# Optimization experiments

Measured on AMD Instinct MI355X. Metric: run time of the kernel, lower is better.

The kernel has to match this reference:

```python
import jax, jax.numpy as jnp
import numpy as np

N_U = 20000; N_I = 20000; D = 256
NNZ = 600000; EGG = 300000; EDD = 300000; B = 8192
DROP = 0.1; LAM2 = 1e-7


def _attention(x, W, a, edges):
    # GAT-style attention over sampled relationship edges (src -> tgt).
    n, d = x.shape
    h = x @ W                                  # [n, d]
    src, tgt = edges[0], edges[1]
    e = jax.nn.leaky_relu((h @ a[:d])[src] + (h @ a[d:])[tgt], 0.2)  # [E]
    m = jax.ops.segment_max(e, tgt, num_segments=n)
    m = jnp.where(jnp.isfinite(m), m, 0.0)
    ex = jnp.exp(e - m[tgt])
    denom = jax.ops.segment_sum(ex, tgt, num_segments=n)             # [n]
    num = jax.ops.segment_sum(ex[:, None] * h[src], tgt, num_segments=n)  # [n, d]
    return num / (denom[:, None] + 1e-9)


def _spmm(rows, cols, vals, x, n_out):
    # sparse [n_out, n_in] @ dense [n_in, d]
    return jax.ops.segment_sum(vals[:, None] * x[cols], rows, num_segments=n_out)


def _mlp(x, W1, b1, W2, b2, W3, b3):
    h = jax.nn.relu(x @ W1 + b1)
    h = jax.nn.relu(h @ W2 + b2)
    return (h @ W3 + b3)[..., 0]


def setup_inputs() -> dict:
    key = jax.random.key(0)
    ks = jax.random.split(key, 24)
    s = 0.02
    inp = {
        'E_g_0': jax.random.normal(ks[0], (N_U, D), jnp.float32) * s,
        'E_d_0': jax.random.normal(ks[1], (N_I, D), jnp.float32) * s,
        'att_W': jax.random.normal(ks[2], (D, D), jnp.float32) * s,
        'att_a': jax.random.normal(ks[3], (2 * D,), jnp.float32) * s,
        'att1_W': jax.random.normal(ks[4], (D, D), jnp.float32) * s,
        'att1_a': jax.random.normal(ks[5], (2 * D,), jnp.float32) * s,
        'W1': jax.random.normal(ks[6], (2 * D, D), jnp.float32) * s,
        'b1': jnp.zeros((D,), jnp.float32),
        'W2': jax.random.normal(ks[7], (D, D), jnp.float32) * s,
        'b2': jnp.zeros((D,), jnp.float32),
        'W3': jax.random.normal(ks[8], (D, 1), jnp.float32) * s,
        'b3': jnp.zeros((1,), jnp.float32),
        'M1': jax.random.normal(ks[9], (2 * D, D), jnp.float32) * s,
        'mb1': jnp.zeros((D,), jnp.float32),
        'M2': jax.random.normal(ks[10], (D, D), jnp.float32) * s,
        'mb2': jnp.zeros((D,), jnp.float32),
        'adj_vals': jax.random.uniform(ks[11], (NNZ,), jnp.float32),
        'uids': jax.random.randint(ks[12], (B,), 0, N_U, jnp.int32),
        'iids': jax.random.randint(ks[13], (B,), 0, N_I, jnp.int32),
        'pos': jax.random.randint(ks[14], (B,), 0, N_I, jnp.int32),
        'neg': jax.random.randint(ks[15], (B,), 0, N_I, jnp.int32),
        'gene_edges': jax.random.randint(ks[16], (2, EGG), 0, N_U, jnp.int32),
        'drug_edges': jax.random.randint(ks[17], (2, EDD), 0, N_I, jnp.int32),
        'adj_rows': jax.random.randint(ks[18], (NNZ,), 0, N_U, jnp.int32),
        'adj_cols': jax.random.randint(ks[19], (NNZ,), 0, N_I, jnp.int32),
        'drop1': jax.random.bernoulli(ks[20], 1.0 - DROP, (NNZ,)),
        'drop2': jax.random.bernoulli(ks[21], 1.0 - DROP, (NNZ,)),
    }
    return inp


def reference(E_g_0, E_d_0, att_W, att_a, att1_W, att1_a, W1, b1, W2, b2, W3, b3,
              M1, mb1, M2, mb2, adj_vals, uids, iids, pos, neg,
              gene_edges, drug_edges, adj_rows, adj_cols, drop1, drop2):
    # Attention-modulated layer-0 embeddings
    E_d0 = 0.1 * _attention(E_d_0, att_W, att_a, drug_edges) + E_d_0
    E_g0 = 0.1 * _attention(E_g_0, att_W, att_a, gene_edges) + E_g_0

    # sparse_dropout + spmm (two independent dropout draws, as in the source)
    scale = 1.0 / (1.0 - DROP)
    v1 = adj_vals * drop1.astype(adj_vals.dtype) * scale
    v2 = adj_vals * drop2.astype(adj_vals.dtype) * scale
    E_g = _spmm(adj_rows, adj_cols, v1, E_d0, N_U)   # adj @ E_d0
    E_d = _spmm(adj_cols, adj_rows, v2, E_g0, N_I)   # adj.T @ E_g0

    u = E_g[uids]; p = E_d[pos]; ng = E_d[neg]
    pos_s = _mlp(jnp.concatenate([u, p], axis=-1), W1, b1, W2, b2, W3, b3)
    neg_s = _mlp(jnp.concatenate([u, ng], axis=-1), W1, b1, W2, b2, W3, b3)

    # BCE-with-logits (labels 1 for pos, 0 for neg) + BPR term
    loss_pos = jnp.mean(jax.nn.softplus(-pos_s))
    loss_neg = jnp.mean(jax.nn.softplus(neg_s))
    loss_bpr = jnp.mean(jax.nn.softplus(-(pos_s - neg_s)))
    loss_r = loss_pos + loss_neg + loss_bpr

    params = (E_g_0, E_d_0, att_W, att_a, att1_W, att1_a,
              W1, b1, W2, b2, W3, b3, M1, mb1, M2, mb2)
    loss_reg = LAM2 * sum(jnp.sum(p_ * p_) for p_ in params)

    loss = loss_reg + loss_r  # loss_s == 0
    return jnp.stack([loss, loss_r, jnp.zeros((), loss.dtype)])
```

## Files before the change

### kernel.cpp

```cpp
#include <hip/hip_runtime.h>
#include <math.h>

#define N_NODES 20000
#define D       256
#define NNZ     600000
#define NEDGE   300000
#define BATCH   8192
#define DROP_SCALE (1.0f/0.9f)
#define LAM2_F  1e-7f

#define M_PAD   20096
#define CSTRIDE 20032

#define C_ATT 56
#define C_ADJ 80

#define BINW 320
#define NBIN 63
#define TILE_E 2048
#define EPT 8
#define T_ATT ((NEDGE + TILE_E - 1) / TILE_E)
#define T_ADJ ((NNZ + TILE_E - 1) / TILE_E)
#define NBLK_P1 (2 * T_ATT + 2 * T_ADJ)
#define CAP_BIN_ATT 5376
#define CAP_BIN_ADJ 6144

#define FP8_SCALE 256.0f
#define VSCALE    58980.0f
#define INV_VSCALE (1.0f/58980.0f)

typedef unsigned short u16;
typedef unsigned char  u8;
typedef __attribute__((ext_vector_type(8))) short bf16x8;
typedef __attribute__((ext_vector_type(4))) float f32x4;
typedef __attribute__((ext_vector_type(2))) float f32x2;
typedef __attribute__((ext_vector_type(4))) unsigned v4u;

__device__ inline float wave_reduce(float v) {
    #pragma unroll
    for (int off = 32; off > 0; off >>= 1) v += __shfl_down(v, off, 64);
    return v;
}

__device__ inline float softplus_f(float x) {
    float r = log1pf(__expf(-fabsf(x)));
    return x > 0.f ? x + r : r;
}

__device__ inline u16 f2bf(float f) {
    unsigned u = __float_as_uint(f);
    unsigned r = u + 0x7fff + ((u >> 16) & 1);
    return (u16)(r >> 16);
}
__device__ inline float bf2f(u16 b) { return __uint_as_float(((unsigned)b) << 16); }

__device__ inline u16 f2h(float f) {
    _Float16 h = (_Float16)f;
    return __builtin_bit_cast(u16, h);
}
__device__ inline float h2f(u16 b) {
    return (float)__builtin_bit_cast(_Float16, b);
}

__device__ inline unsigned f32x4_to_fp8x4(float a, float b, float c, float d) {
    int r = 0;
    r = __builtin_amdgcn_cvt_pk_fp8_f32(a, b, r, false);
    r = __builtin_amdgcn_cvt_pk_fp8_f32(c, d, r, true);
    return (unsigned)r;
}
__device__ inline u8 f32_to_fp8(float a) {
    int r = __builtin_amdgcn_cvt_pk_fp8_f32(a, a, 0, false);
    return (u8)(r & 0xff);
}

__device__ inline void gld_lds16(const void* g, void* l) {
    __builtin_amdgcn_global_load_lds((const __attribute__((address_space(1))) void*)g,
                                     (__attribute__((address_space(3))) void*)l, 16, 0, 0);
}

struct RegArgs { const float* p[14]; int n[14]; };

__global__ __launch_bounds__(256) void init_kernel(const unsigned char* __restrict__ drop,
                                                   const int* __restrict__ uids, const int* __restrict__ pos,
                                                   const int* __restrict__ neg,
                                                   const float* __restrict__ att_W, const float* __restrict__ att_a,
                                                   float* __restrict__ wlv, float* __restrict__ wrv,
                                                   unsigned* __restrict__ bm2, unsigned* __restrict__ bm3,
                                                   unsigned int* __restrict__ flag) {
    if (blockIdx.x < 96) {
        int i = blockIdx.x * blockDim.x + threadIdx.x;
        if (i < BATCH) {
            int v = uids[i];
            atomicOr(&bm2[v >> 5], 1u << (v & 31));
        } else if (i < 2 * BATCH) {
            int v = pos[i - BATCH];
            atomicOr(&bm3[v >> 5], 1u << (v & 31));
        } else {
            int v = neg[i - 2 * BATCH];
            atomicOr(&bm3[v >> 5], 1u << (v & 31));
        }
    } else if (blockIdx.x == 96) {
        __shared__ int cnt_s;
        if (threadIdx.x == 0) cnt_s = 0;
        __syncthreads();
        int c = 0;
        for (int i = threadIdx.x; i < 1024; i += blockDim.x)
            if (drop[4*i + 1] != 0) c++;
        atomicAdd(&cnt_s, c);
        __syncthreads();
        if (threadIdx.x == 0) *flag = (cnt_s > 64) ? 1u : 0u;
    } else {
        int t = threadIdx.x;
        float s1 = 0.f, s2 = 0.f;
        for (int n = 0; n < D; n++) {
            float w = att_W[(size_t)t * D + n];
            s1 += w * att_a[n];
            s2 += w * att_a[D + n];
        }
        wlv[t] = s1; wrv[t] = s2;
    }
}

#define NB_CAST (2 * M_PAD / 4)
#define NB_T1   (D * D / 256)
#define NB_T2   (2 * D * D / 256)
#define NB_T3   (D * D / 256)
#define NB_PREP (NB_CAST + NB_T1 + NB_T2 + NB_T3)
#define NB_REG  448
__global__ __launch_bounds__(256) void p1prep_kernel(
        const int* __restrict__ dtgt, const int* __restrict__ dsrc,
        const int* __restrict__ gtgt, const int* __restrict__ gsrc,
        const int* __restrict__ ar,   const int* __restrict__ ac,
        const float* __restrict__ vals,
        const void* __restrict__ drop1, const void* __restrict__ drop2,
        const unsigned int* __restrict__ flag,
        const unsigned* __restrict__ bm2, const unsigned* __restrict__ bm3,
        int* __restrict__ pcur, unsigned* __restrict__ attbin, uint2* __restrict__ adjbin,
        const float* __restrict__ E_g, const float* __restrict__ E_d,
        u16* __restrict__ Eg_bf, u16* __restrict__ Ed_bf,
        const float* __restrict__ att_W,
        const float* __restrict__ W1, const float* __restrict__ W2,
        u16* __restrict__ attWT, u16* __restrict__ W1T, u16* __restrict__ W2T,
        const float* __restrict__ wlv, const float* __restrict__ wrv,
        float* __restrict__ hl_g, float* __restrict__ hr_g,
        float* __restrict__ hl_d, float* __restrict__ hr_d,
        float* __restrict__ regp, RegArgs ra, float* __restrict__ acc) {
    if (blockIdx.x < NBLK_P1) {
        __shared__ int hist[NBIN];
        __shared__ int basep[NBIN];
        for (int i = threadIdx.x; i < NBIN; i += 256) hist[i] = 0;
        __syncthreads();

        int b = blockIdx.x;
        int s, t0;
        if (b < T_ATT)               { s = 0; t0 = b; }
        else if (b < 2 * T_ATT)      { s = 1; t0 = b - T_ATT; }
        else if (b < 2*T_ATT + T_ADJ){ s = 2; t0 = b - 2 * T_ATT; }
        else                         { s = 3; t0 = b - 2 * T_ATT - T_ADJ; }
        int base = t0 * TILE_E;
        int regN = (s < 2) ? NEDGE : NNZ;

        int bins[EPT], rank[EPT];
        unsigned key[EPT], pay[EPT];
        float pv[EPT];

        if (s < 2) {
            const int* tgt = (s == 0) ? dtgt : gtgt;
            const int* src = (s == 0) ? dsrc : gsrc;
            #pragma unroll
            for (int e = 0; e < EPT; e++) {
                int idx = base + e * 256 + threadIdx.x;
                rank[e] = -1;
                if (idx < regN) {
                    int k = __builtin_nontemporal_load(tgt + idx);
                    int sv = __builtin_nontemporal_load(src + idx);
                    key[e] = (unsigned)k; pay[e] = (unsigned)sv;
                    bins[e] = k / BINW;
                    rank[e] = atomicAdd(&hist[bins[e]], 1);
                }
            }
        } else {
            const unsigned int bf = *flag;
            const int* keyp = (s == 2) ? ar : ac;
            const int* othp = (s == 2) ? ac : ar;
            const void* drp = (s == 2) ? drop1 : drop2;
            const unsigned* bm = (s == 2) ? bm2 : bm3;
            #pragma unroll
            for (int e = 0; e < EPT; e++) {
                int idx = base + e * 256 + threadIdx.x;
                rank[e] = -1;
                if (idx < regN) {
                    int k = __builtin_nontemporal_load(keyp + idx);
                    if ((bm[k >> 5] >> (k & 31)) & 1) {
                        bool keep = bf ? (__builtin_nontemporal_load((const u8*)drp + idx) != 0)
                                       : (__builtin_nontemporal_load((const unsigned*)drp + idx) != 0);
                        if (keep) {
                            float v = __builtin_nontemporal_load(vals + idx) * DROP_SCALE;
                            int oth = __builtin_nontemporal_load(othp + idx);
                            key[e] = (unsigned)k; pay[e] = (unsigned)oth; pv[e] = v;
                            bins[e] = k / BINW;
                            rank[e] = atomicAdd(&hist[bins[e]], 1);
                        }
                    }
                }
            }
        }
        __syncthreads();
        for (int i = threadIdx.x; i < NBIN; i += 256) {
            int h = hist[i];
            basep[i] = h ? atomicAdd(&pcur[s * NBIN + i], h) : 0;
        }
        __syncthreads();
        if (s < 2) {
            unsigned* seg = attbin + (size_t)s * NBIN * CAP_BIN_ATT;
            #pragma unroll
            for (int e = 0; e < EPT; e++) {
                if (rank[e] < 0) continue;
                int pos = basep[bins[e]] + rank[e];
                if (pos < CAP_BIN_ATT)
                    seg[(size_t)bins[e] * CAP_BIN_ATT + pos] = key[e] | (pay[e] << 16);
            }
        } else {
            uint2* seg = adjbin + (size_t)(s - 2) * NBIN * CAP_BIN_ADJ;
            #pragma unroll
            for (int e = 0; e < EPT; e++) {
                if (rank[e] < 0) continue;
                int pos = basep[bins[e]] + rank[e];
                if (pos < CAP_BIN_ADJ) {
                    uint2 pr; pr.x = key[e] | (pay[e] << 16); pr.y = __float_as_uint(pv[e]);
                    seg[(size_t)bins[e] * CAP_BIN_ADJ + pos] = pr;
                }
            }
        }
    } else {
        int bid = blockIdx.x - NBLK_P1;
        int w = threadIdx.x >> 6, lane = threadIdx.x & 63;
        if (bid < NB_CAST) {
            int wid  = (bid * 256 + threadIdx.x) >> 6;
            int is_d = (wid >= M_PAD);
            int row  = is_d ? wid - M_PAD : wid;
            u16* dst = (is_d ? Ed_bf : Eg_bf) + (size_t)row * D;
            float s3 = 0.f;
            if (row >= N_NODES) {
                ((ushort4*)dst)[lane] = make_ushort4(0, 0, 0, 0);
            } else {
                const float* src = (is_d ? E_d : E_g) + (size_t)row * D;
                float4 e  = ((const float4*)src)[lane];
                float4 l4 = ((const float4*)wlv)[lane];
                float4 r4 = ((const float4*)wrv)[lane];
                ((ushort4*)dst)[lane] = make_ushort4(f2bf(e.x), f2bf(e.y), f2bf(e.z), f2bf(e.w));
                float s1 = e.x*l4.x + e.y*l4.y + e.z*l4.z + e.w*l4.w;
                float s2 = e.x*r4.x + e.y*r4.y + e.z*r4.z + e.w*r4.w;
                s3 = e.x*e.x + e.y*e.y + e.z*e.z + e.w*e.w;
                s1 = wave_reduce(s1); s2 = wave_reduce(s2);
                if (lane == 0) {
                    if (is_d) { hl_d[row] = s1; hr_d[row] = s2; }
                    else      { hl_g[row] = s1; hr_g[row] = s2; }
                }
            }
            s3 = wave_reduce(s3);
            __shared__ float sm3[4];
            if (lane == 0) sm3[threadIdx.x >> 6] = s3;
            __syncthreads();
            if (threadIdx.x == 0) regp[bid] = sm3[0] + sm3[1] + sm3[2] + sm3[3];
        } else if (bid < NB_CAST + NB_T1) {
            int o = (bid - NB_CAST) * 256 + threadIdx.x;
            int n = o >> 8, k = o & 255;
            attWT[o] = f2bf(att_W[(size_t)k * D + n]);
        } else if (bid < NB_CAST + NB_T1 + NB_T2) {
            int o = (bid - NB_CAST - NB_T1) * 256 + threadIdx.x;
            int n = o / (2 * D), k = o - n * (2 * D);
            W1T[o] = f2bf(W1[(size_t)k * D + n]);
        } else if (bid < NB_PREP) {
            int o = (bid - NB_CAST - NB_T1 - NB_T2) * 256 + threadIdx.x;
            int n = o >> 8, k = o & 255;
            W2T[o] = f2bf(W2[(size_t)k * D + n]);
        } else {
            int rb = bid - NB_PREP;
            const float* p = ra.p[rb >> 5];
            int n = ra.n[rb >> 5];
            int base = (rb & 31) * 4096;
            if (base >= n) return;
            float sum = 0.f;
            if (base + 4096 <= n) {
                const float4* p4 = (const float4*)(p + base);
                float4 v = p4[threadIdx.x];
                sum += v.x*v.x + v.y*v.y + v.z*v.z + v.w*v.w;
                v = p4[256 + threadIdx.x];
                sum += v.x*v.x + v.y*v.y + v.z*v.z + v.w*v.w;
                v = p4[512 + threadIdx.x];
                sum += v.x*v.x + v.y*v.y + v.z*v.z + v.w*v.w;
                v = p4[768 + threadIdx.x];
                sum += v.x*v.x + v.y*v.y + v.z*v.z + v.w*v.w;
            } else {
                for (int i = base + threadIdx.x; i < n; i += 256) { float v = p[i]; sum += v * v; }
            }
            sum = wave_reduce(sum);
            __shared__ float smr[4];
            if (lane == 0) smr[w] = sum;
            __syncthreads();
            if (threadIdx.x == 0)
                atomicAdd(&acc[0], smr[0] + smr[1] + smr[2] + smr[3]);
        }
    }
}

#define NB_P2   (4 * NBIN)
#define NB_ATTG ((M_PAD / 128) * 4)
__global__ __launch_bounds__(256) void p2gemm_kernel(
        const int* __restrict__ pcur, const unsigned* __restrict__ attbin,
        const uint2* __restrict__ adjbin,
        const float* __restrict__ hl_d, const float* __restrict__ hr_d,
        const float* __restrict__ hl_g, const float* __restrict__ hr_g,
        int* __restrict__ cnt, unsigned* __restrict__ srcs, unsigned* __restrict__ adj,
        const u16* __restrict__ Eg_bf, const u16* __restrict__ Ed_bf,
        const u16* __restrict__ attWT, u8* __restrict__ h_g, u8* __restrict__ h_d) {
    if (blockIdx.x < NB_P2) {
        int s   = blockIdx.x / NBIN;
        int bin = blockIdx.x - s * NBIN;
        int nodeBase = bin * BINW;
        __shared__ int cur[BINW];
        for (int t = threadIdx.x; t < BINW; t += 256) cur[t] = 0;
        __syncthreads();
        if (s < 2) {
            int m = pcur[s * NBIN + bin]; if (m > CAP_BIN_ATT) m = CAP_BIN_ATT;
            const unsigned* seg = attbin + ((size_t)s * NBIN + bin) * CAP_BIN_ATT;
            const float* hl = (s == 0) ? hl_d : hl_g;
            const float* hr = (s == 0) ? hr_d : hr_g;
            for (int k = threadIdx.x; k < m; k += 256) {
                unsigned e = seg[k];
                int lk  = (int)(e & 0xFFFFu) - nodeBase;
                int src = (int)(e >> 16);
                float ev = hl[src] + hr[nodeBase + lk];
                ev = ev > 0.f ? ev : 0.2f * ev;
                u16 xh = f2h(__expf(ev));
                int c = atomicAdd(&cur[lk], 1);
                if (c < C_ATT)
                    srcs[(size_t)s * N_NODES * C_ATT + (size_t)(nodeBase + lk) * C_ATT + c] =
                        (unsigned)src | ((unsigned)xh << 16);
            }
            __syncthreads();
            for (int t = threadIdx.x; t < BINW; t += 256) {
                int node = nodeBase + t;
                if (node < N_NODES) {
                    int n = cur[t]; if (n > C_ATT) n = C_ATT;
                    cnt[s * CSTRIDE + node] = n;
                }
            }
        } else {
            int m = pcur[s * NBIN + bin]; if (m > CAP_BIN_ADJ) m = CAP_BIN_ADJ;
            const uint2* seg = adjbin + ((size_t)(s - 2) * NBIN + bin) * CAP_BIN_ADJ;
            for (int k = threadIdx.x; k < m; k += 256) {
                uint2 e = seg[k];
                int lk  = (int)(e.x & 0xFFFFu) - nodeBase;
                int oth = (int)(e.x >> 16);
                float v = __uint_as_float(e.y);
                unsigned pk = ((unsigned)(v * VSCALE + 0.5f) << 16) | (unsigned)oth;
                int c = atomicAdd(&cur[lk], 1);
                if (c < C_ADJ)
                    adj[(size_t)(s - 2) * N_NODES * C_ADJ + (size_t)(nodeBase + lk) * C_ADJ + c] = pk;
            }
            __syncthreads();
            for (int t = threadIdx.x; t < BINW; t += 256) {
                int node = nodeBase + t;
                if (node < N_NODES) {
                    int n = cur[t]; if (n > C_ADJ) n = C_ADJ;
                    cnt[s * CSTRIDE + node] = n;
                }
            }
        }
    } else {
        int t  = blockIdx.x - NB_P2;
        int z  = t / (2 * (M_PAD / 128));
        int r  = t - z * (2 * (M_PAD / 128));
        int by = r / (M_PAD / 128);
        int bx = r - by * (M_PAD / 128);
        const u16* A = z ? Ed_bf : Eg_bf;
        u8* C = z ? h_d : h_g;
        __shared__ __align__(16) short As[128][32];
        __shared__ __align__(16) short Bs[128][32];
        int tid = threadIdx.x;
        int wave = tid >> 6, lane = tid & 63;
        int bm = bx * 128, bn = by * 128;
        int sr = lane >> 2;
        int sc = (lane & 3) * 8;

        f32x4 acc[4][4];
        #pragma unroll
        for (int i = 0; i < 4; i++)
            #pragma unroll
            for (int j = 0; j < 4; j++)
                #pragma unroll
                for (int q = 0; q < 4; q++) acc[i][j][q] = 0.f;

        int wr = (wave >> 1) * 64;
        int wc = (wave & 1) * 64;
        int fr = lane & 15;
        int fk = (lane >> 4) * 8;

        for (int k0 = 0; k0 < D; k0 += 32) {
            #pragma unroll
            for (int j = 0; j < 2; j++) {
                int r0 = wave * 32 + j * 16;
                gld_lds16(A     + (size_t)(bm + r0 + sr) * D + k0 + sc, &As[r0][0]);
                gld_lds16(attWT + (size_t)(bn + r0 + sr) * D + k0 + sc, &Bs[r0][0]);
            }
            __syncthreads();
            bf16x8 af[4], bfr[4];
            #pragma unroll
            for (int i = 0; i < 4; i++) af[i]  = *(const bf16x8*)&As[wr + i*16 + fr][fk];
            #pragma unroll
            for (int j = 0; j < 4; j++) bfr[j] = *(const bf16x8*)&Bs[wc + j*16 + fr][fk];
            #pragma unroll
            for (int i = 0; i < 4; i++)
                #pragma unroll
                for (int j = 0; j < 4; j++)
                    acc[i][j] = __builtin_amdgcn_mfma_f32_16x16x32_bf16(af[i], bfr[j], acc[i][j], 0, 0, 0);
            __syncthreads();
        }

        #pragma unroll
        for (int j = 0; j < 4; j++) {
            int col = bn + wc + j * 16 + fr;
            #pragma unroll
            for (int i = 0; i < 4; i++) {
                #pragma unroll
                for (int q = 0; q < 4; q++) {
                    int row = bm + wr + i * 16 + (lane >> 4) * 4 + q;
                    if (row < N_NODES)
                        C[(size_t)row * D + col] = f32_to_fp8(acc[i][j][q] * FP8_SCALE);
                }
            }
        }
    }
}

__global__ __launch_bounds__(256) void gemm_bf16(const u16* __restrict__ A, const u16* __restrict__ BT,
                                                 void* __restrict__ C, int M, int N, int K,
                                                 const float* __restrict__ bias, int do_relu, int out_mode,
                                                 const float* __restrict__ w3) {
    __shared__ __align__(16) short As[128][32];
    __shared__ __align__(16) short Bs[128][32];
    int tid = threadIdx.x;
    int wave = tid >> 6, lane = tid & 63;
    int bm = blockIdx.x * 128, bn = blockIdx.y * 128;
    int sr = lane >> 2;
    int sc = (lane & 3) * 8;

    f32x4 acc[4][4];
    #pragma unroll
    for (int i = 0; i < 4; i++)
        #pragma unroll
        for (int j = 0; j < 4; j++)
            #pragma unroll
            for (int r = 0; r < 4; r++) acc[i][j][r] = 0.f;

    int wr = (wave >> 1) * 64;
    int wc = (wave & 1) * 64;
    int fr = lane & 15;
    int fk = (lane >> 4) * 8;

    for (int k0 = 0; k0 < K; k0 += 32) {
        #pragma unroll
        for (int j = 0; j < 2; j++) {
            int r0 = wave * 32 + j * 16;
            gld_lds16(A  + (size_t)(bm + r0 + sr) * K + k0 + sc, &As[r0][0]);
            gld_lds16(BT + (size_t)(bn + r0 + sr) * K + k0 + sc, &Bs[r0][0]);
        }
        __syncthreads();
        bf16x8 af[4], bfr[4];
        #pragma unroll
        for (int i = 0; i < 4; i++) af[i]  = *(const bf16x8*)&As[wr + i*16 + fr][fk];
        #pragma unroll
        for (int j = 0; j < 4; j++) bfr[j] = *(const bf16x8*)&Bs[wc + j*16 + fr][fk];
        #pragma unroll
        for (int i = 0; i < 4; i++)
            #pragma unroll
            for (int j = 0; j < 4; j++)
                acc[i][j] = __builtin_amdgcn_mfma_f32_16x16x32_bf16(af[i], bfr[j], acc[i][j], 0, 0, 0);
        __syncthreads();
    }

    if (out_mode == 2) {
        __shared__ float sacc[128];
        for (int t = tid; t < 128; t += 256) sacc[t] = 0.f;
        __syncthreads();
        float bvj[4], w3j[4];
        #pragma unroll
        for (int j = 0; j < 4; j++) {
            int col = bn + wc + j * 16 + fr;
            bvj[j] = bias[col];
            w3j[j] = w3[col];
        }
        #pragma unroll
        for (int i = 0; i < 4; i++) {
            #pragma unroll
            for (int r = 0; r < 4; r++) {
                float rs = 0.f;
                #pragma unroll
                for (int j = 0; j < 4; j++) {
                    float v = fmaxf(acc[i][j][r] + bvj[j], 0.f);
                    rs += v * w3j[j];
                }
                rs += __shfl_xor(rs, 1, 64);
                rs += __shfl_xor(rs, 2, 64);
                rs += __shfl_xor(rs, 4, 64);
                rs += __shfl_xor(rs, 8, 64);
                if (fr == 0)
                    atomicAdd(&sacc[wr + i * 16 + (lane >> 4) * 4 + r], rs);
            }
        }
        __syncthreads();
        float* sb = (float*)C;
        for (int t = tid; t < 128; t += 256)
            atomicAdd(&sb[bm + t], sacc[t]);
        return;
    }

    #pragma unroll
    for (int j = 0; j < 4; j++) {
        int col = bn + wc + j * 16 + fr;
        float bv = bias ? bias[col] : 0.f;
        #pragma unroll
        for (int i = 0; i < 4; i++) {
            #pragma unroll
            for (int r = 0; r < 4; r++) {
                int row = bm + wr + i * 16 + (lane >> 4) * 4 + r;
                if (row < M) {
                    float v = acc[i][j][r] + bv;
                    if (do_relu) v = fmaxf(v, 0.f);
                    ((u16*)C)[(size_t)row * N + col] = f2bf(v);
                }
            }
        }
    }
}

__global__ __launch_bounds__(256) void att_kernel(const u8* __restrict__ h_d, const u8* __restrict__ h_g,
                                                  const int* __restrict__ cur, const unsigned* __restrict__ srcs,
                                                  const u16* __restrict__ Ed_bf, const u16* __restrict__ Eg_bf,
                                                  u8* __restrict__ E_d0p, u8* __restrict__ E_g0p) {
    int wid  = (blockIdx.x * blockDim.x + threadIdx.x) >> 6;
    int lane = threadIdx.x & 63;
    if (wid >= 2 * N_NODES) return;
    int is_g = (wid >= N_NODES);
    int node = is_g ? wid - N_NODES : wid;
    const unsigned* h32 = (const unsigned*)(is_g ? h_g : h_d);
    int reg = is_g ? 1 : 0;
    const unsigned* sv = srcs + (size_t)reg * N_NODES * C_ATT + (size_t)node * C_ATT;
    int n = cur[reg * CSTRIDE + node];
    if (n > C_ATT) n = C_ATT;
    float ax = 0.f, ay = 0.f, az = 0.f, aw = 0.f, denom = 0.f;
    int k = 0;
    for (; k + 8 <= n; k += 8) {
        v4u qa = __builtin_nontemporal_load((const v4u*)(sv + k));
        v4u qb = __builtin_nontemporal_load((const v4u*)(sv + k + 4));
        unsigned g[8]; float x[8];
        #pragma unroll
        for (int j = 0; j < 4; j++) {
            g[j]     = h32[((size_t)(qa[j] & 0xFFFFu) << 6) + lane];
            g[4 + j] = h32[((size_t)(qb[j] & 0xFFFFu) << 6) + lane];
            x[j]     = h2f((u16)(qa[j] >> 16));
            x[4 + j] = h2f((u16)(qb[j] >> 16));
        }
        #pragma unroll
        for (int j = 0; j < 8; j++) {
            denom += x[j];
            f32x2 lo = __builtin_amdgcn_cvt_pk_f32_fp8(g[j], false);
            f32x2 hi = __builtin_amdgcn_cvt_pk_f32_fp8(g[j], true);
            ax += x[j]*lo[0]; ay += x[j]*lo[1]; az += x[j]*hi[0]; aw += x[j]*hi[1];
        }
    }
    for (; k + 4 <= n; k += 4) {
        v4u qa = __builtin_nontemporal_load((const v4u*)(sv + k));
        unsigned g[4]; float x[4];
        #pragma unroll
        for (int j = 0; j < 4; j++) {
            g[j] = h32[((size_t)(qa[j] & 0xFFFFu) << 6) + lane];
            x[j] = h2f((u16)(qa[j] >> 16));
        }
        #pragma unroll
        for (int j = 0; j < 4; j++) {
            denom += x[j];
            f32x2 lo = __builtin_amdgcn_cvt_pk_f32_fp8(g[j], false);
            f32x2 hi = __builtin_amdgcn_cvt_pk_f32_fp8(g[j], true);
            ax += x[j]*lo[0]; ay += x[j]*lo[1]; az += x[j]*hi[0]; aw += x[j]*hi[1];
        }
    }
    for (; k < n; k++) {
        unsigned q = sv[k];
        float xv = h2f((u16)(q >> 16));
        unsigned g = h32[((size_t)(q & 0xFFFFu) << 6) + lane];
        denom += xv;
        f32x2 lo = __builtin_amdgcn_cvt_pk_f32_fp8(g, false);
        f32x2 hi = __builtin_amdgcn_cvt_pk_f32_fp8(g, true);
        ax += xv*lo[0]; ay += xv*lo[1]; az += xv*hi[0]; aw += xv*hi[1];
    }
    float sc = 0.1f / (denom + 1e-9f);
    const u16* E0b = is_g ? Eg_bf : Ed_bf;
    u8*       out  = is_g ? E_g0p : E_d0p;
    ushort4 b4 = ((const ushort4*)(E0b + (size_t)node * D))[lane];
    unsigned pk = f32x4_to_fp8x4(FP8_SCALE * bf2f(b4.x) + sc * ax, FP8_SCALE * bf2f(b4.y) + sc * ay,
                                 FP8_SCALE * bf2f(b4.z) + sc * az, FP8_SCALE * bf2f(b4.w) + sc * aw);
    ((unsigned*)(out + (size_t)node * D))[lane] = pk;
}

__global__ __launch_bounds__(256) void pull_kernel(const int* __restrict__ uids, const int* __restrict__ pos,
                                                   const int* __restrict__ neg,
                                                   const int* __restrict__ cur, const unsigned* __restrict__ adj,
                                                   const u8* __restrict__ E_d0p, const u8* __restrict__ E_g0p,
                                                   u16* __restrict__ X) {
    int wid  = (blockIdx.x * blockDim.x + threadIdx.x) >> 6;
    int lane = threadIdx.x & 63;
    if (wid >= 3 * BATCH) return;
    int type = wid >> 13;
    int b    = wid & (BATCH - 1);
    int node, reg; const u8* E;
    if (type == 0)      { node = uids[b]; reg = 2; E = E_d0p; }
    else if (type == 1) { node = pos[b];  reg = 3; E = E_g0p; }
    else                { node = neg[b];  reg = 3; E = E_g0p; }
    const unsigned* E32 = (const unsigned*)E;
    const unsigned* av = adj + (size_t)(reg - 2) * N_NODES * C_ADJ + (size_t)node * C_ADJ;
    int n = cur[reg * CSTRIDE + node];
    if (n > C_ADJ) n = C_ADJ;
    float ax = 0.f, ay = 0.f, az = 0.f, aw = 0.f;
    int k = 0;
    for (; k + 8 <= n; k += 8) {
        v4u qa = __builtin_nontemporal_load((const v4u*)(av + k));
        v4u qb = __builtin_nontemporal_load((const v4u*)(av + k + 4));
        unsigned g[8]; float v[8];
        #pragma unroll
        for (int j = 0; j < 4; j++) {
            g[j]     = E32[((size_t)(qa[j] & 0xFFFFu) << 6) + lane];
            g[4 + j] = E32[((size_t)(qb[j] & 0xFFFFu) << 6) + lane];
            v[j]     = (float)(qa[j] >> 16) * INV_VSCALE;
            v[4 + j] = (float)(qb[j] >> 16) * INV_VSCALE;
        }
        #pragma unroll
        for (int j = 0; j < 8; j++) {
            f32x2 lo = __builtin_amdgcn_cvt_pk_f32_fp8(g[j], false);
            f32x2 hi = __builtin_amdgcn_cvt_pk_f32_fp8(g[j], true);
            ax += v[j]*lo[0]; ay += v[j]*lo[1]; az += v[j]*hi[0]; aw += v[j]*hi[1];
        }
    }
    for (; k + 4 <= n; k += 4) {
        v4u qa = __builtin_nontemporal_load((const v4u*)(av + k));
        unsigned g[4]; float v[4];
        #pragma unroll
        for (int j = 0; j < 4; j++) {
            g[j] = E32[((size_t)(qa[j] & 0xFFFFu) << 6) + lane];
            v[j] = (float)(qa[j] >> 16) * INV_VSCALE;
        }
        #pragma unroll
        for (int j = 0; j < 4; j++) {
            f32x2 lo = __builtin_amdgcn_cvt_pk_f32_fp8(g[j], false);
            f32x2 hi = __builtin_amdgcn_cvt_pk_f32_fp8(g[j], true);
            ax += v[j]*lo[0]; ay += v[j]*lo[1]; az += v[j]*hi[0]; aw += v[j]*hi[1];
        }
    }
    for (; k < n; k++) {
        unsigned q = av[k];
        int c = q & 0xFFFF;
        float v = (float)(q >> 16) * INV_VSCALE;
        unsigned g = E32[((size_t)c << 6) + lane];
        f32x2 lo = __builtin_amdgcn_cvt_pk_f32_fp8(g, false);
        f32x2 hi = __builtin_amdgcn_cvt_pk_f32_fp8(g, true);
        ax += v*lo[0]; ay += v*lo[1]; az += v*hi[0]; aw += v*hi[1];
    }
    const float inv = 1.0f / FP8_SCALE;
    ushort4 r = make_ushort4(f2bf(ax * inv), f2bf(ay * inv), f2bf(az * inv), f2bf(aw * inv));
    if (type == 0) {
        ((ushort4*)(X + (size_t)b * 2 * D))[lane] = r;
        ((ushort4*)(X + (size_t)(BATCH + b) * 2 * D))[lane] = r;
    } else if (type == 1) {
        ((ushort4*)(X + (size_t)b * 2 * D + D))[lane] = r;
    } else {
        ((ushort4*)(X + (size_t)(BATCH + b) * 2 * D + D))[lane] = r;
    }
}

#define NB_TAIL 16
__global__ __launch_bounds__(256) void tail_kernel(const float* __restrict__ s,
                                                   const float* __restrict__ b3p,
                                                   const float* __restrict__ regp,
                                                   float* __restrict__ acc, float* __restrict__ out) {
    int bid = blockIdx.x, tid = threadIdx.x;
    int w = tid >> 6, lane = tid & 63;
    float b3 = b3p[0];
    float lp = 0.f, ln = 0.f, lb = 0.f, rsum = 0.f;
    for (int i = bid * 256 + tid; i < BATCH; i += NB_TAIL * 256) {
        float ps = s[i] + b3, ns = s[BATCH + i] + b3;
        lp += softplus_f(-ps);
        ln += softplus_f(ns);
        lb += softplus_f(-(ps - ns));
    }
    for (int i = bid * 256 + tid; i < NB_CAST; i += NB_TAIL * 256) rsum += regp[i];
    lp = wave_reduce(lp); ln = wave_reduce(ln); lb = wave_reduce(lb); rsum = wave_reduce(rsum);
    __shared__ float sm[4][4];
    if (lane == 0) { sm[0][w] = lp; sm[1][w] = ln; sm[2][w] = lb; sm[3][w] = rsum; }
    __syncthreads();
    if (tid == 0) {
        float a = 0.f, b = 0.f, c = 0.f, rg = 0.f;
        for (int i = 0; i < 4; i++) { a += sm[0][i]; b += sm[1][i]; c += sm[2][i]; rg += sm[3][i]; }
        atomicAdd(&acc[1], a); atomicAdd(&acc[2], b); atomicAdd(&acc[3], c);
        atomicAdd(&acc[0], rg);
    }
    __syncthreads();
    __shared__ int lastf;
    if (tid == 0) {
        __threadfence();
        unsigned t = atomicAdd((unsigned*)&acc[8], 1u);
        lastf = (t == NB_TAIL - 1);
    }
    __syncthreads();
    if (!lastf || tid != 0) return;
    float a0 = __hip_atomic_load(&acc[0], __ATOMIC_RELAXED, __HIP_MEMORY_SCOPE_AGENT);
    float a1 = __hip_atomic_load(&acc[1], __ATOMIC_RELAXED, __HIP_MEMORY_SCOPE_AGENT);
    float a2 = __hip_atomic_load(&acc[2], __ATOMIC_RELAXED, __HIP_MEMORY_SCOPE_AGENT);
    float a3 = __hip_atomic_load(&acc[3], __ATOMIC_RELAXED, __HIP_MEMORY_SCOPE_AGENT);
    float lr = (a1 + a2 + a3) * (1.0f / (float)BATCH);
    out[0] = LAM2_F * a0 + lr;
    out[1] = lr;
    out[2] = 0.f;
}

extern "C" void kernel_launch(void* const* d_in, const int* in_sizes, int n_in,
                              void* d_out, int out_size, void* d_ws, size_t ws_size,
                              hipStream_t stream) {
    (void)n_in; (void)out_size; (void)ws_size;
    const float* E_g_0   = (const float*)d_in[0];
    const float* E_d_0   = (const float*)d_in[1];
    const float* att_W   = (const float*)d_in[2];
    const float* att_a   = (const float*)d_in[3];
    const float* W1      = (const float*)d_in[6];
    const float* b1      = (const float*)d_in[7];
    const float* W2      = (const float*)d_in[8];
    const float* b2      = (const float*)d_in[9];
    const float* W3      = (const float*)d_in[10];
    const float* b3      = (const float*)d_in[11];
    const float* adj_vals= (const float*)d_in[16];
    const int*   uids    = (const int*)d_in[17];
    const int*   pos     = (const int*)d_in[19];
    const int*   neg     = (const int*)d_in[20];
    const int*   gene_e  = (const int*)d_in[21];
    const int*   drug_e  = (const int*)d_in[22];
    const int*   adj_rows= (const int*)d_in[23];
    const int*   adj_cols= (const int*)d_in[24];
    const void*  drop1   = d_in[25];
    const void*  drop2   = d_in[26];

    char* ws = (char*)d_ws;
    size_t cur_off = 0;
    auto take = [&](size_t bytes) -> void* {
        void* p = ws + cur_off;
        cur_off += (bytes + 255) & ~(size_t)255;
        return p;
    };
    u16* Eg_bf = (u16*)take((size_t)M_PAD * D * 2);
    u16* Ed_bf = (u16*)take((size_t)M_PAD * D * 2);
    u16* X     = Eg_bf;
    u16* attWT = (u16*)take((size_t)D * D * 2);
    u16* W1T   = (u16*)take((size_t)D * 2 * D * 2);
    u16* W2T   = (u16*)take((size_t)D * D * 2);
    u8*  h_g   = (u8*)take((size_t)M_PAD * D);
    u8*  h_d   = (u8*)take((size_t)M_PAD * D);
    u8*  E_g0p = (u8*)take((size_t)N_NODES * D);
    u8*  E_d0p = (u8*)take((size_t)N_NODES * D);
    u16* H1    = (u16*)take((size_t)2 * BATCH * D * 2);
    float* hl_g = (float*)take((size_t)N_NODES * 4);
    float* hr_g = (float*)take((size_t)N_NODES * 4);
    float* hl_d = (float*)take((size_t)N_NODES * 4);
    float* hr_d = (float*)take((size_t)N_NODES * 4);
    float* wlv  = (float*)take((size_t)D * 4);
    float* wrv  = (float*)take((size_t)D * 4);
    float* regp = (float*)take((size_t)NB_CAST * 4);
    unsigned* srcs = (unsigned*)take((size_t)2 * N_NODES * C_ATT * 4);
    unsigned* adj  = (unsigned*)take((size_t)2 * N_NODES * C_ADJ * 4);
    int*   cnt  = (int*)take((size_t)4 * CSTRIDE * 4);
    unsigned* attbin = (unsigned*)take((size_t)2 * NBIN * CAP_BIN_ATT * 4);
    uint2*    adjbin = (uint2*)take((size_t)2 * NBIN * CAP_BIN_ADJ * 8);
    int*      pcur = (int*)take((size_t)4 * NBIN * 4);
    unsigned* bm2  = (unsigned*)take(4096);
    unsigned* bm3  = (unsigned*)take(4096);
    float*    acc  = (float*)take(256);
    float*    sbuf = (float*)take((size_t)2 * BATCH * 4);
    size_t zbytes = (char*)sbuf + (size_t)2 * BATCH * 4 - (char*)pcur;

    hipMemsetAsync(pcur, 0, zbytes, stream);
    init_kernel<<<98, 256, 0, stream>>>((const unsigned char*)drop1, uids, pos, neg,
                                        att_W, att_a, wlv, wrv,
                                        bm2, bm3, (unsigned int*)(acc + 4));

    RegArgs ra;
    for (int i = 0; i < 14; i++) { ra.p[i] = (const float*)d_in[i + 2]; ra.n[i] = in_sizes[i + 2]; }
    p1prep_kernel<<<NBLK_P1 + NB_PREP + NB_REG, 256, 0, stream>>>(
        drug_e + NEDGE, drug_e, gene_e + NEDGE, gene_e,
        adj_rows, adj_cols, adj_vals, drop1, drop2,
        (const unsigned int*)(acc + 4), bm2, bm3,
        pcur, attbin, adjbin,
        E_g_0, E_d_0, Eg_bf, Ed_bf, att_W, W1, W2,
        attWT, W1T, W2T, wlv, wrv, hl_g, hr_g, hl_d, hr_d, regp, ra, acc);

    p2gemm_kernel<<<NB_P2 + NB_ATTG, 256, 0, stream>>>(
        pcur, attbin, adjbin, hl_d, hr_d, hl_g, hr_g, cnt, srcs, adj,
        Eg_bf, Ed_bf, attWT, h_g, h_d);

    att_kernel<<<10000, 256, 0, stream>>>(h_d, h_g, cnt, srcs,
                                          Ed_bf, Eg_bf, E_d0p, E_g0p);

    pull_kernel<<<6144, 256, 0, stream>>>(uids, pos, neg, cnt, adj, E_d0p, E_g0p, X);

    gemm_bf16<<<dim3(2 * BATCH / 128, 2, 1), 256, 0, stream>>>(
        X, W1T, H1, 2 * BATCH, D, 2 * D, b1, 1, 0, nullptr);
    gemm_bf16<<<dim3(2 * BATCH / 128, 2, 1), 256, 0, stream>>>(
        H1, W2T, sbuf, 2 * BATCH, D, D, b2, 1, 2, W3);

    tail_kernel<<<NB_TAIL, 256, 0, stream>>>(sbuf, b3, regp, acc, (float*)d_out);
}
```

Measured before the change: 297.6 us.

## Fuse MLP GEMMs and loss tail into one kernel, drop batch bitmaps

The two MLP GEMM launches and the loss tail launch are merged into a single kernel. Its stages are chained by per-row-tile atomic counters with spin-waits. The memset and the bitmap/flag init work are folded into a single-block init kernel that zeroes the scratch and computes the attention projection vectors. The adjacency binning no longer filters edges by the uid/pos/neg bitmaps, so every kept edge is binned, and the bin capacity is raised to fit. The dropout-format detection moves into each block via a ballot. This removes launches and bitmap work but adds more binned edges, and the spin-waits depend on the producer blocks being scheduled before the consumers.

```diff
diff --git a/kernel.cpp b/kernel.cpp
--- a/kernel.cpp
+++ b/kernel.cpp
@@ -23,7 +23,7 @@
 #define T_ADJ ((NNZ + TILE_E - 1) / TILE_E)
 #define NBLK_P1 (2 * T_ATT + 2 * T_ADJ)
 #define CAP_BIN_ATT 5376
-#define CAP_BIN_ADJ 6144
+#define CAP_BIN_ADJ 9216
 
 #define FP8_SCALE 256.0f
 #define VSCALE    58980.0f
@@ -80,44 +80,54 @@
 
 struct RegArgs { const float* p[14]; int n[14]; };
 
-__global__ __launch_bounds__(256) void init_kernel(const unsigned char* __restrict__ drop,
-                                                   const int* __restrict__ uids, const int* __restrict__ pos,
-                                                   const int* __restrict__ neg,
-                                                   const float* __restrict__ att_W, const float* __restrict__ att_a,
-                                                   float* __restrict__ wlv, float* __restrict__ wrv,
-                                                   unsigned* __restrict__ bm2, unsigned* __restrict__ bm3,
-                                                   unsigned int* __restrict__ flag) {
-    if (blockIdx.x < 96) {
-        int i = blockIdx.x * blockDim.x + threadIdx.x;
-        if (i < BATCH) {
-            int v = uids[i];
-            atomicOr(&bm2[v >> 5], 1u << (v & 31));
-        } else if (i < 2 * BATCH) {
-            int v = pos[i - BATCH];
-            atomicOr(&bm3[v >> 5], 1u << (v & 31));
-        } else {
-            int v = neg[i - 2 * BATCH];
-            atomicOr(&bm3[v >> 5], 1u << (v & 31));
-        }
-    } else if (blockIdx.x == 96) {
-        __shared__ int cnt_s;
-        if (threadIdx.x == 0) cnt_s = 0;
-        __syncthreads();
-        int c = 0;
-        for (int i = threadIdx.x; i < 1024; i += blockDim.x)
-            if (drop[4*i + 1] != 0) c++;
-        atomicAdd(&cnt_s, c);
-        __syncthreads();
-        if (threadIdx.x == 0) *flag = (cnt_s > 64) ? 1u : 0u;
-    } else {
-        int t = threadIdx.x;
-        float s1 = 0.f, s2 = 0.f;
-        for (int n = 0; n < D; n++) {
-            float w = att_W[(size_t)t * D + n];
-            s1 += w * att_a[n];
-            s2 += w * att_a[D + n];
-        }
-        wlv[t] = s1; wrv[t] = s2;
+__device__ inline void gemm_tile_k(const u16* __restrict__ A, const u16* __restrict__ BT, int K,
+                                   int bm, int bn, short (*As)[32], short (*Bs)[32],
+                                   f32x4 (&acr)[4][4]) {
+    int tid = threadIdx.x, wave = tid >> 6, lane = tid & 63;
+    int sr = lane >> 2, sc = (lane & 3) * 8;
+    int wr = (wave >> 1) * 64, wc = (wave & 1) * 64;
+    int fr = lane & 15, fk = (lane >> 4) * 8;
+    for (int k0 = 0; k0 < K; k0 += 32) {
+        #pragma unroll
+        for (int j = 0; j < 2; j++) {
+            int r0 = wave * 32 + j * 16;
+            gld_lds16(A  + (size_t)(bm + r0 + sr) * K + k0 + sc, &As[r0][0]);
+            gld_lds16(BT + (size_t)(bn + r0 + sr) * K + k0 + sc, &Bs[r0][0]);
+        }
+        __syncthreads();
+        bf16x8 af[4], bfr[4];
+        #pragma unroll
+        for (int i = 0; i < 4; i++) af[i]  = *(const bf16x8*)&As[wr + i*16 + fr][fk];
+        #pragma unroll
+        for (int j = 0; j < 4; j++) bfr[j] = *(const bf16x8*)&Bs[wc + j*16 + fr][fk];
+        #pragma unroll
+        for (int i = 0; i < 4; i++)
+            #pragma unroll
+            for (int j = 0; j < 4; j++)
+                acr[i][j] = __builtin_amdgcn_mfma_f32_16x16x32_bf16(af[i], bfr[j], acr[i][j], 0, 0, 0);
+        __syncthreads();
+    }
+}
+
+__global__ __launch_bounds__(1024) void init_kernel(const float* __restrict__ att_W,
+                                                    const float* __restrict__ att_a,
+                                                    float* __restrict__ wlv, float* __restrict__ wrv,
+                                                    int* __restrict__ zbase, int zwords) {
+    int tid = threadIdx.x;
+    for (int i = tid; i < zwords; i += 1024) zbase[i] = 0;
+    int t = tid & 255, q = tid >> 8;
+    float s1 = 0.f, s2 = 0.f;
+    for (int n = q * 64; n < q * 64 + 64; n++) {
+        float w = att_W[(size_t)t * D + n];
+        s1 += w * att_a[n];
+        s2 += w * att_a[D + n];
+    }
+    __shared__ float r1[4][256], r2[4][256];
+    r1[q][t] = s1; r2[q][t] = s2;
+    __syncthreads();
+    if (q == 0) {
+        wlv[t] = r1[0][t] + r1[1][t] + r1[2][t] + r1[3][t];
+        wrv[t] = r2[0][t] + r2[1][t] + r2[2][t] + r2[3][t];
     }
 }
 
@@ -133,8 +143,6 @@
         const int* __restrict__ ar,   const int* __restrict__ ac,
         const float* __restrict__ vals,
         const void* __restrict__ drop1, const void* __restrict__ drop2,
-        const unsigned int* __restrict__ flag,
-        const unsigned* __restrict__ bm2, const unsigned* __restrict__ bm3,
         int* __restrict__ pcur, unsigned* __restrict__ attbin, uint2* __restrict__ adjbin,
         const float* __restrict__ E_g, const float* __restrict__ E_d,
         u16* __restrict__ Eg_bf, u16* __restrict__ Ed_bf,
@@ -180,27 +188,25 @@
                 }
             }
         } else {
-            const unsigned int bf = *flag;
             const int* keyp = (s == 2) ? ar : ac;
             const int* othp = (s == 2) ? ac : ar;
             const void* drp = (s == 2) ? drop1 : drop2;
-            const unsigned* bm = (s == 2) ? bm2 : bm3;
+            bool nzs = ((const u8*)drp)[4 * threadIdx.x + 1] != 0;
+            const bool bf = __popcll(__ballot(nzs)) > 16;
             #pragma unroll
             for (int e = 0; e < EPT; e++) {
                 int idx = base + e * 256 + threadIdx.x;
                 rank[e] = -1;
                 if (idx < regN) {
-                    int k = __builtin_nontemporal_load(keyp + idx);
-                    if ((bm[k >> 5] >> (k & 31)) & 1) {
-                        bool keep = bf ? (__builtin_nontemporal_load((const u8*)drp + idx) != 0)
-                                       : (__builtin_nontemporal_load((const unsigned*)drp + idx) != 0);
-                        if (keep) {
-                            float v = __builtin_nontemporal_load(vals + idx) * DROP_SCALE;
-                            int oth = __builtin_nontemporal_load(othp + idx);
-                            key[e] = (unsigned)k; pay[e] = (unsigned)oth; pv[e] = v;
-                            bins[e] = k / BINW;
-                            rank[e] = atomicAdd(&hist[bins[e]], 1);
-                        }
+                    bool keep = bf ? (__builtin_nontemporal_load((const u8*)drp + idx) != 0)
+                                   : (__builtin_nontemporal_load((const unsigned*)drp + idx) != 0);
+                    if (keep) {
+                        int k = __builtin_nontemporal_load(keyp + idx);
+                        float v = __builtin_nontemporal_load(vals + idx) * DROP_SCALE;
+                        int oth = __builtin_nontemporal_load(othp + idx);
+                        key[e] = (unsigned)k; pay[e] = (unsigned)oth; pv[e] = v;
+                        bins[e] = k / BINW;
+                        rank[e] = atomicAdd(&hist[bins[e]], 1);
                     }
                 }
             }
@@ -379,46 +385,17 @@
         u8* C = z ? h_d : h_g;
         __shared__ __align__(16) short As[128][32];
         __shared__ __align__(16) short Bs[128][32];
-        int tid = threadIdx.x;
-        int wave = tid >> 6, lane = tid & 63;
+        int wave = threadIdx.x >> 6, lane = threadIdx.x & 63;
         int bm = bx * 128, bn = by * 128;
-        int sr = lane >> 2;
-        int sc = (lane & 3) * 8;
-
-        f32x4 acc[4][4];
+        f32x4 acr[4][4];
         #pragma unroll
         for (int i = 0; i < 4; i++)
             #pragma unroll
             for (int j = 0; j < 4; j++)
                 #pragma unroll
-                for (int q = 0; q < 4; q++) acc[i][j][q] = 0.f;
-
-        int wr = (wave >> 1) * 64;
-        int wc = (wave & 1) * 64;
-        int fr = lane & 15;
-        int fk = (lane >> 4) * 8;
-
-        for (int k0 = 0; k0 < D; k0 += 32) {
-            #pragma unroll
-            for (int j = 0; j < 2; j++) {
-                int r0 = wave * 32 + j * 16;
-                gld_lds16(A     + (size_t)(bm + r0 + sr) * D + k0 + sc, &As[r0][0]);
-                gld_lds16(attWT + (size_t)(bn + r0 + sr) * D + k0 + sc, &Bs[r0][0]);
-            }
-            __syncthreads();
-            bf16x8 af[4], bfr[4];
-            #pragma unroll
-            for (int i = 0; i < 4; i++) af[i]  = *(const bf16x8*)&As[wr + i*16 + fr][fk];
-            #pragma unroll
-            for (int j = 0; j < 4; j++) bfr[j] = *(const bf16x8*)&Bs[wc + j*16 + fr][fk];
-            #pragma unroll
-            for (int i = 0; i < 4; i++)
-                #pragma unroll
-                for (int j = 0; j < 4; j++)
-                    acc[i][j] = __builtin_amdgcn_mfma_f32_16x16x32_bf16(af[i], bfr[j], acc[i][j], 0, 0, 0);
-            __syncthreads();
-        }
-
+                for (int q = 0; q < 4; q++) acr[i][j][q] = 0.f;
+        gemm_tile_k(A, attWT, D, bm, bn, As, Bs, acr);
+        int wr = (wave >> 1) * 64, wc = (wave & 1) * 64, fr = lane & 15;
         #pragma unroll
         for (int j = 0; j < 4; j++) {
             int col = bn + wc + j * 16 + fr;
@@ -428,108 +405,7 @@
                 for (int q = 0; q < 4; q++) {
                     int row = bm + wr + i * 16 + (lane >> 4) * 4 + q;
                     if (row < N_NODES)
-                        C[(size_t)row * D + col] = f32_to_fp8(acc[i][j][q] * FP8_SCALE);
-                }
-            }
-        }
-    }
-}
-
-__global__ __launch_bounds__(256) void gemm_bf16(const u16* __restrict__ A, const u16* __restrict__ BT,
-                                                 void* __restrict__ C, int M, int N, int K,
-                                                 const float* __restrict__ bias, int do_relu, int out_mode,
-                                                 const float* __restrict__ w3) {
-    __shared__ __align__(16) short As[128][32];
-    __shared__ __align__(16) short Bs[128][32];
-    int tid = threadIdx.x;
-    int wave = tid >> 6, lane = tid & 63;
-    int bm = blockIdx.x * 128, bn = blockIdx.y * 128;
-    int sr = lane >> 2;
-    int sc = (lane & 3) * 8;
-
-    f32x4 acc[4][4];
-    #pragma unroll
-    for (int i = 0; i < 4; i++)
-        #pragma unroll
-        for (int j = 0; j < 4; j++)
-            #pragma unroll
-            for (int r = 0; r < 4; r++) acc[i][j][r] = 0.f;
-
-    int wr = (wave >> 1) * 64;
-    int wc = (wave & 1) * 64;
-    int fr = lane & 15;
-    int fk = (lane >> 4) * 8;
-
-    for (int k0 = 0; k0 < K; k0 += 32) {
-        #pragma unroll
-        for (int j = 0; j < 2; j++) {
-            int r0 = wave * 32 + j * 16;
-            gld_lds16(A  + (size_t)(bm + r0 + sr) * K + k0 + sc, &As[r0][0]);
-            gld_lds16(BT + (size_t)(bn + r0 + sr) * K + k0 + sc, &Bs[r0][0]);
-        }
-        __syncthreads();
-        bf16x8 af[4], bfr[4];
-        #pragma unroll
-        for (int i = 0; i < 4; i++) af[i]  = *(const bf16x8*)&As[wr + i*16 + fr][fk];
-        #pragma unroll
-        for (int j = 0; j < 4; j++) bfr[j] = *(const bf16x8*)&Bs[wc + j*16 + fr][fk];
-        #pragma unroll
-        for (int i = 0; i < 4; i++)
-            #pragma unroll
-            for (int j = 0; j < 4; j++)
-                acc[i][j] = __builtin_amdgcn_mfma_f32_16x16x32_bf16(af[i], bfr[j], acc[i][j], 0, 0, 0);
-        __syncthreads();
-    }
-
-    if (out_mode == 2) {
-        __shared__ float sacc[128];
-        for (int t = tid; t < 128; t += 256) sacc[t] = 0.f;
-        __syncthreads();
-        float bvj[4], w3j[4];
-        #pragma unroll
-        for (int j = 0; j < 4; j++) {
-            int col = bn + wc + j * 16 + fr;
-            bvj[j] = bias[col];
-            w3j[j] = w3[col];
-        }
-        #pragma unroll
-        for (int i = 0; i < 4; i++) {
-            #pragma unroll
-            for (int r = 0; r < 4; r++) {
-                float rs = 0.f;
-                #pragma unroll
-                for (int j = 0; j < 4; j++) {
-                    float v = fmaxf(acc[i][j][r] + bvj[j], 0.f);
-                    rs += v * w3j[j];
-                }
-                rs += __shfl_xor(rs, 1, 64);
-                rs += __shfl_xor(rs, 2, 64);
-                rs += __shfl_xor(rs, 4, 64);
-                rs += __shfl_xor(rs, 8, 64);
-                if (fr == 0)
-                    atomicAdd(&sacc[wr + i * 16 + (lane >> 4) * 4 + r], rs);
-            }
-        }
-        __syncthreads();
-        float* sb = (float*)C;
-        for (int t = tid; t < 128; t += 256)
-            atomicAdd(&sb[bm + t], sacc[t]);
-        return;
-    }
-
-    #pragma unroll
-    for (int j = 0; j < 4; j++) {
-        int col = bn + wc + j * 16 + fr;
-        float bv = bias ? bias[col] : 0.f;
-        #pragma unroll
-        for (int i = 0; i < 4; i++) {
-            #pragma unroll
-            for (int r = 0; r < 4; r++) {
-                int row = bm + wr + i * 16 + (lane >> 4) * 4 + r;
-                if (row < M) {
-                    float v = acc[i][j][r] + bv;
-                    if (do_relu) v = fmaxf(v, 0.f);
-                    ((u16*)C)[(size_t)row * N + col] = f2bf(v);
+                        C[(size_t)row * D + col] = f32_to_fp8(acr[i][j][q] * FP8_SCALE);
                 }
             }
         }
@@ -679,49 +555,137 @@
     }
 }
 
-#define NB_TAIL 16
-__global__ __launch_bounds__(256) void tail_kernel(const float* __restrict__ s,
-                                                   const float* __restrict__ b3p,
-                                                   const float* __restrict__ regp,
-                                                   float* __restrict__ acc, float* __restrict__ out) {
+#define MLP_NB (256 + 128 + 16)
+__global__ __launch_bounds__(256) void mlp_kernel(
+        const u16* __restrict__ X, const u16* __restrict__ W1T,
+        u16* __restrict__ H1, const u16* __restrict__ W2T,
+        const float* __restrict__ b1, const float* __restrict__ b2,
+        const float* __restrict__ W3, const float* __restrict__ b3p,
+        const float* __restrict__ regp, float* __restrict__ sbuf,
+        float* __restrict__ acc, int* __restrict__ syn, float* __restrict__ out) {
     int bid = blockIdx.x, tid = threadIdx.x;
-    int w = tid >> 6, lane = tid & 63;
-    float b3 = b3p[0];
-    float lp = 0.f, ln = 0.f, lb = 0.f, rsum = 0.f;
-    for (int i = bid * 256 + tid; i < BATCH; i += NB_TAIL * 256) {
-        float ps = s[i] + b3, ns = s[BATCH + i] + b3;
-        lp += softplus_f(-ps);
-        ln += softplus_f(ns);
-        lb += softplus_f(-(ps - ns));
-    }
-    for (int i = bid * 256 + tid; i < NB_CAST; i += NB_TAIL * 256) rsum += regp[i];
-    lp = wave_reduce(lp); ln = wave_reduce(ln); lb = wave_reduce(lb); rsum = wave_reduce(rsum);
-    __shared__ float sm[4][4];
-    if (lane == 0) { sm[0][w] = lp; sm[1][w] = ln; sm[2][w] = lb; sm[3][w] = rsum; }
-    __syncthreads();
-    if (tid == 0) {
-        float a = 0.f, b = 0.f, c = 0.f, rg = 0.f;
-        for (int i = 0; i < 4; i++) { a += sm[0][i]; b += sm[1][i]; c += sm[2][i]; rg += sm[3][i]; }
-        atomicAdd(&acc[1], a); atomicAdd(&acc[2], b); atomicAdd(&acc[3], c);
-        atomicAdd(&acc[0], rg);
-    }
-    __syncthreads();
-    __shared__ int lastf;
-    if (tid == 0) {
+    int wave = tid >> 6, lane = tid & 63;
+    __shared__ __align__(16) short As[128][32];
+    __shared__ __align__(16) short Bs[128][32];
+    __shared__ float sacc[128];
+    if (bid < 256) {
+        int bx = bid & 127, by = bid >> 7;
+        int bm = bx * 128, bn = by * 128;
+        f32x4 acr[4][4];
+        #pragma unroll
+        for (int i = 0; i < 4; i++)
+            #pragma unroll
+            for (int j = 0; j < 4; j++)
+                #pragma unroll
+                for (int q = 0; q < 4; q++) acr[i][j][q] = 0.f;
+        gemm_tile_k(X, W1T, 2 * D, bm, bn, As, Bs, acr);
+        int wr = (wave >> 1) * 64, wc = (wave & 1) * 64, fr = lane & 15;
+        #pragma unroll
+        for (int j = 0; j < 4; j++) {
+            int col = bn + wc + j * 16 + fr;
+            float bv = b1[col];
+            #pragma unroll
+            for (int i = 0; i < 4; i++) {
+                #pragma unroll
+                for (int q = 0; q < 4; q++) {
+                    int row = bm + wr + i * 16 + (lane >> 4) * 4 + q;
+                    H1[(size_t)row * D + col] = f2bf(fmaxf(acr[i][j][q] + bv, 0.f));
+                }
+            }
+        }
         __threadfence();
-        unsigned t = atomicAdd((unsigned*)&acc[8], 1u);
-        lastf = (t == NB_TAIL - 1);
-    }
-    __syncthreads();
-    if (!lastf || tid != 0) return;
-    float a0 = __hip_atomic_load(&acc[0], __ATOMIC_RELAXED, __HIP_MEMORY_SCOPE_AGENT);
-    float a1 = __hip_atomic_load(&acc[1], __ATOMIC_RELAXED, __HIP_MEMORY_SCOPE_AGENT);
-    float a2 = __hip_atomic_load(&acc[2], __ATOMIC_RELAXED, __HIP_MEMORY_SCOPE_AGENT);
-    float a3 = __hip_atomic_load(&acc[3], __ATOMIC_RELAXED, __HIP_MEMORY_SCOPE_AGENT);
-    float lr = (a1 + a2 + a3) * (1.0f / (float)BATCH);
-    out[0] = LAM2_F * a0 + lr;
-    out[1] = lr;
-    out[2] = 0.f;
+        if (tid == 0) atomicAdd(&syn[bx], 1);
+    } else if (bid < 384) {
+        int x = bid - 256, bm = x * 128;
+        if (tid == 0) {
+            while (__hip_atomic_load(&syn[x], __ATOMIC_ACQUIRE, __HIP_MEMORY_SCOPE_AGENT) < 2)
+                __builtin_amdgcn_s_sleep(8);
+        }
+        __syncthreads();
+        for (int t = tid; t < 128; t += 256) sacc[t] = 0.f;
+        __syncthreads();
+        int wr = (wave >> 1) * 64, wc = (wave & 1) * 64, fr = lane & 15;
+        for (int bn = 0; bn < 256; bn += 128) {
+            f32x4 acr[4][4];
+            #pragma unroll
+            for (int i = 0; i < 4; i++)
+                #pragma unroll
+                for (int j = 0; j < 4; j++)
+                    #pragma unroll
+                    for (int q = 0; q < 4; q++) acr[i][j][q] = 0.f;
+            gemm_tile_k(H1, W2T, D, bm, bn, As, Bs, acr);
+            float bvj[4], w3j[4];
+            #pragma unroll
+            for (int j = 0; j < 4; j++) {
+                int col = bn + wc + j * 16 + fr;
+                bvj[j] = b2[col];
+                w3j[j] = W3[col];
+            }
+            #pragma unroll
+            for (int i = 0; i < 4; i++) {
+                #pragma unroll
+                for (int q = 0; q < 4; q++) {
+                    float rs = 0.f;
+                    #pragma unroll
+                    for (int j = 0; j < 4; j++)
+                        rs += fmaxf(acr[i][j][q] + bvj[j], 0.f) * w3j[j];
+                    rs += __shfl_xor(rs, 1, 64);
+                    rs += __shfl_xor(rs, 2, 64);
+                    rs += __shfl_xor(rs, 4, 64);
+                    rs += __shfl_xor(rs, 8, 64);
+                    if (fr == 0)
+                        atomicAdd(&sacc[wr + i * 16 + (lane >> 4) * 4 + q], rs);
+                }
+            }
+            __syncthreads();
+        }
+        for (int t = tid; t < 128; t += 256) sbuf[bm + t] = sacc[t];
+        __threadfence();
+        if (tid == 0) atomicAdd(&syn[128], 1);
+    } else {
+        int tb = bid - 384;
+        if (tid == 0) {
+            while (__hip_atomic_load(&syn[128], __ATOMIC_ACQUIRE, __HIP_MEMORY_SCOPE_AGENT) < 128)
+                __builtin_amdgcn_s_sleep(16);
+        }
+        __syncthreads();
+        float b3 = b3p[0];
+        float lp = 0.f, ln = 0.f, lb = 0.f, rsum = 0.f;
+        for (int i = tb * 256 + tid; i < BATCH; i += 16 * 256) {
+            float ps = sbuf[i] + b3, ns = sbuf[BATCH + i] + b3;
+            lp += softplus_f(-ps);
+            ln += softplus_f(ns);
+            lb += softplus_f(-(ps - ns));
+        }
+        for (int i = tb * 256 + tid; i < NB_CAST; i += 16 * 256) rsum += regp[i];
+        lp = wave_reduce(lp); ln = wave_reduce(ln); lb = wave_reduce(lb); rsum = wave_reduce(rsum);
+        __shared__ float sm[4][4];
+        if (lane == 0) { sm[0][wave] = lp; sm[1][wave] = ln; sm[2][wave] = lb; sm[3][wave] = rsum; }
+        __syncthreads();
+        if (tid == 0) {
+            float a = 0.f, b = 0.f, c = 0.f, rg = 0.f;
+            for (int i = 0; i < 4; i++) { a += sm[0][i]; b += sm[1][i]; c += sm[2][i]; rg += sm[3][i]; }
+            atomicAdd(&acc[1], a); atomicAdd(&acc[2], b); atomicAdd(&acc[3], c);
+            atomicAdd(&acc[0], rg);
+        }
+        __syncthreads();
+        __shared__ int lastf;
+        if (tid == 0) {
+            __threadfence();
+            int t = atomicAdd(&syn[129], 1);
+            lastf = (t == 15);
+        }
+        __syncthreads();
+        if (!lastf || tid != 0) return;
+        float a0 = __hip_atomic_load(&acc[0], __ATOMIC_RELAXED, __HIP_MEMORY_SCOPE_AGENT);
+        float a1 = __hip_atomic_load(&acc[1], __ATOMIC_RELAXED, __HIP_MEMORY_SCOPE_AGENT);
+        float a2 = __hip_atomic_load(&acc[2], __ATOMIC_RELAXED, __HIP_MEMORY_SCOPE_AGENT);
+        float a3 = __hip_atomic_load(&acc[3], __ATOMIC_RELAXED, __HIP_MEMORY_SCOPE_AGENT);
+        float lr = (a1 + a2 + a3) * (1.0f / (float)BATCH);
+        out[0] = LAM2_F * a0 + lr;
+        out[1] = lr;
+        out[2] = 0.f;
+    }
 }
 
 extern "C" void kernel_launch(void* const* d_in, const int* in_sizes, int n_in,
@@ -774,29 +738,24 @@
     float* wlv  = (float*)take((size_t)D * 4);
     float* wrv  = (float*)take((size_t)D * 4);
     float* regp = (float*)take((size_t)NB_CAST * 4);
+    float* sbuf = (float*)take((size_t)2 * BATCH * 4);
     unsigned* srcs = (unsigned*)take((size_t)2 * N_NODES * C_ATT * 4);
     unsigned* adj  = (unsigned*)take((size_t)2 * N_NODES * C_ADJ * 4);
     int*   cnt  = (int*)take((size_t)4 * CSTRIDE * 4);
     unsigned* attbin = (unsigned*)take((size_t)2 * NBIN * CAP_BIN_ATT * 4);
     uint2*    adjbin = (uint2*)take((size_t)2 * NBIN * CAP_BIN_ADJ * 8);
     int*      pcur = (int*)take((size_t)4 * NBIN * 4);
-    unsigned* bm2  = (unsigned*)take(4096);
-    unsigned* bm3  = (unsigned*)take(4096);
     float*    acc  = (float*)take(256);
-    float*    sbuf = (float*)take((size_t)2 * BATCH * 4);
-    size_t zbytes = (char*)sbuf + (size_t)2 * BATCH * 4 - (char*)pcur;
-
-    hipMemsetAsync(pcur, 0, zbytes, stream);
-    init_kernel<<<98, 256, 0, stream>>>((const unsigned char*)drop1, uids, pos, neg,
-                                        att_W, att_a, wlv, wrv,
-                                        bm2, bm3, (unsigned int*)(acc + 4));
+    int*      syn  = (int*)take(1024);
+    int zwords = (int)((((char*)syn + 1024) - (char*)pcur) / 4);
+
+    init_kernel<<<1, 1024, 0, stream>>>(att_W, att_a, wlv, wrv, pcur, zwords);
 
     RegArgs ra;
     for (int i = 0; i < 14; i++) { ra.p[i] = (const float*)d_in[i + 2]; ra.n[i] = in_sizes[i + 2]; }
     p1prep_kernel<<<NBLK_P1 + NB_PREP + NB_REG, 256, 0, stream>>>(
         drug_e + NEDGE, drug_e, gene_e + NEDGE, gene_e,
         adj_rows, adj_cols, adj_vals, drop1, drop2,
-        (const unsigned int*)(acc + 4), bm2, bm3,
         pcur, attbin, adjbin,
         E_g_0, E_d_0, Eg_bf, Ed_bf, att_W, W1, W2,
         attWT, W1T, W2T, wlv, wrv, hl_g, hr_g, hl_d, hr_d, regp, ra, acc);
@@ -810,10 +769,6 @@
 
     pull_kernel<<<6144, 256, 0, stream>>>(uids, pos, neg, cnt, adj, E_d0p, E_g0p, X);
 
-    gemm_bf16<<<dim3(2 * BATCH / 128, 2, 1), 256, 0, stream>>>(
-        X, W1T, H1, 2 * BATCH, D, 2 * D, b1, 1, 0, nullptr);
-    gemm_bf16<<<dim3(2 * BATCH / 128, 2, 1), 256, 0, stream>>>(
-        H1, W2T, sbuf, 2 * BATCH, D, D, b2, 1, 2, W3);
-
-    tail_kernel<<<NB_TAIL, 256, 0, stream>>>(sbuf, b3, regp, acc, (float*)d_out);
-}
+    mlp_kernel<<<MLP_NB, 256, 0, stream>>>(X, W1T, H1, W2T, b1, b2, W3, b3,
+                                           regp, sbuf, acc, syn, (float*)d_out);
+}
```

New measurement: 355.6 us. 1.19x slower.
